# Kernel optimization log

Hardware: AMD Instinct MI355X
Metric: run time of the kernel (lower is better)

The kernel has to match this reference:

```python
import jax, jax.numpy as jnp
import numpy as np

KH, KW = 5, 5
LOWER, UPPER = 0.0, 1.0


def setup_inputs() -> dict:
    key = jax.random.key(0)
    k1, k2, k3, k4, k5, k6, k7 = jax.random.split(key, 7)
    T, Cin, H, W = 15, 64, 256, 256
    Cout, Ho, Wo = 128, 252, 252
    K = 16  # kwta winners
    input_spikes = (jax.random.uniform(k1, (T, Cin, H, W)) < 0.1).astype(jnp.float32)
    output_spikes = (jax.random.uniform(k2, (T, Cout, Ho, Wo)) < 0.05).astype(jnp.float32)
    # winners: distinct feature maps (as produced by k-winners-take-all), valid (r, c)
    f = jax.random.permutation(k3, Cout)[:K]
    r = jax.random.randint(k4, (K,), 0, Ho)
    c = jax.random.randint(k5, (K,), 0, Wo)
    winners = jnp.stack([f, r, c], axis=1).astype(jnp.int64)
    weight = 0.8 + 0.02 * jax.random.normal(k6, (Cout, Cin, KH, KW), dtype=jnp.float32)
    ltp = jnp.full((Cout,), 0.004, dtype=jnp.float32)
    ltd = jnp.full((Cout,), -0.003, dtype=jnp.float32)
    return {"input_spikes": input_spikes, "output_spikes": output_spikes,
            "winners": winners, "weight": weight, "ltp": ltp, "ltd": ltd}


def reference(input_spikes, output_spikes, winners, weight, ltp, ltd):
    # latencies: sum of spikes over time  (Cin,H,W) and (Cout,Ho,Wo)
    in_lat = jnp.sum(input_spikes, axis=0)
    out_lat = jnp.sum(output_spikes, axis=0)
    Cin = in_lat.shape[0]

    def pairing(w):
        f, r, c = w[0], w[1], w[2]
        patch = jax.lax.dynamic_slice(in_lat, (0, r, c), (Cin, KH, KW))  # (Cin,KH,KW)
        return patch >= out_lat[f, r, c]

    pairings = jax.vmap(pairing)(winners)  # (K, Cin, KH, KW) bool
    fs = winners[:, 0]
    lr_rows = jnp.where(pairings,
                        ltp[fs][:, None, None, None],
                        ltd[fs][:, None, None, None])  # (K, Cin, KH, KW)
    lr = jnp.zeros_like(weight).at[fs].set(lr_rows)
    stab = (weight - LOWER) * (UPPER - weight)
    new_weight = weight + lr * stab
    return jnp.clip(new_weight, LOWER, UPPER)
```

## Files before the change

### kernel.cpp

```cpp
#include <hip/hip_runtime.h>

#define T_STEPS 15
#define CIN     64
#define H_IN    256
#define W_IN    256
#define COUT    128
#define HO      252
#define WO      252
#define KWIN    16
#define KH      5
#define KW      5
#define LOWERB  0.0f
#define UPPERB  1.0f

#define W_ELEMS (COUT * CIN * KH * KW)

__global__ __launch_bounds__(256) void stdp_update_kernel(
    const float* __restrict__ in_spikes,
    const float* __restrict__ out_spikes,
    const int*   __restrict__ winners,
    const float* __restrict__ weight,
    const float* __restrict__ ltp,
    const float* __restrict__ ltd,
    float*       __restrict__ out)
{
    __shared__ int   wf[KWIN];
    __shared__ int   wr[KWIN];
    __shared__ int   wc[KWIN];
    __shared__ float wol[KWIN];

    const int tid = threadIdx.x;
    if (tid < KWIN) {
        const int f = winners[3 * tid + 0];
        const int r = winners[3 * tid + 1];
        const int c = winners[3 * tid + 2];
        wf[tid] = f; wr[tid] = r; wc[tid] = c;
        size_t base = (size_t)f * (HO * WO) + (size_t)r * WO + (size_t)c;
        float s = 0.0f;
        #pragma unroll
        for (int t = 0; t < T_STEPS; ++t)
            s += out_spikes[base + (size_t)t * (COUT * HO * WO)];
        wol[tid] = s;
    }
    __syncthreads();

    const int idx = blockIdx.x * blockDim.x + tid;
    if (idx >= W_ELEMS) return;

    const int cout = idx / (CIN * KH * KW);
    const int rem  = idx % (CIN * KH * KW);

    int k = -1;
    #pragma unroll
    for (int i = 0; i < KWIN; ++i)
        if (wf[i] == cout) k = i;

    const float w = weight[idx];
    float nw;
    if (k < 0) {
        nw = w;
    } else {
        const int cin = rem / (KH * KW);
        const int p   = rem % (KH * KW);
        const int kh  = p / KW;
        const int kw  = p % KW;
        const int r   = wr[k] + kh;
        const int c   = wc[k] + kw;
        size_t base = (size_t)cin * (H_IN * W_IN) + (size_t)r * W_IN + (size_t)c;
        float s = 0.0f;
        #pragma unroll
        for (int t = 0; t < T_STEPS; ++t)
            s += in_spikes[base + (size_t)t * (CIN * H_IN * W_IN)];
        const float lr = (s >= wol[k]) ? ltp[cout] : ltd[cout];
        nw = w + lr * ((w - LOWERB) * (UPPERB - w));
    }
    nw = fminf(fmaxf(nw, LOWERB), UPPERB);
    out[idx] = nw;
}

extern "C" void kernel_launch(void* const* d_in, const int* in_sizes, int n_in,
                              void* d_out, int out_size, void* d_ws, size_t ws_size,
                              hipStream_t stream) {
    const float* in_spikes  = (const float*)d_in[0];
    const float* out_spikes = (const float*)d_in[1];
    const int*   winners    = (const int*)d_in[2];
    const float* weight     = (const float*)d_in[3];
    const float* ltp        = (const float*)d_in[4];
    const float* ltd        = (const float*)d_in[5];
    float*       out        = (float*)d_out;

    const int block = 256;
    const int grid  = (W_ELEMS + block - 1) / block;
    stdp_update_kernel<<<grid, block, 0, stream>>>(
        in_spikes, out_spikes, winners, weight, ltp, ltd, out);
}
```

Before: 621.3 us.

## Vectorize weight update to float4 and drop shared-memory winner staging

Each thread now handles four consecutive weights through float4 loads and stores, which cuts the grid by four. The block-wide shared-memory stage that summed winner output latencies is replaced: each thread scans the winners array and, only for winning output channels, computes the output latency itself. This removes a barrier and the 15-step strided out_spikes reads that every block used to do, which dominated the runtime because there are thousands of blocks. The trade-off is that winning threads do redundant out_spikes reads and run four gather loops serially.

```diff
diff --git a/kernel.cpp b/kernel.cpp
--- a/kernel.cpp
+++ b/kernel.cpp
@@ -13,9 +13,11 @@
 #define LOWERB  0.0f
 #define UPPERB  1.0f
 
-#define W_ELEMS (COUT * CIN * KH * KW)
+#define CKK     (CIN * KH * KW)
+#define W_ELEMS (COUT * CKK)
+#define NVEC    (W_ELEMS / 4)
 
-__global__ __launch_bounds__(256) void stdp_update_kernel(
+__global__ __launch_bounds__(256) void stdp_update_v2(
     const float* __restrict__ in_spikes,
     const float* __restrict__ out_spikes,
     const int*   __restrict__ winners,
@@ -24,58 +26,58 @@
     const float* __restrict__ ltd,
     float*       __restrict__ out)
 {
-    __shared__ int   wf[KWIN];
-    __shared__ int   wr[KWIN];
-    __shared__ int   wc[KWIN];
-    __shared__ float wol[KWIN];
+    const int g = blockIdx.x * blockDim.x + threadIdx.x;
+    if (g >= NVEC) return;
+    const int idx  = g * 4;
+    const int cout = idx / CKK;
 
-    const int tid = threadIdx.x;
-    if (tid < KWIN) {
-        const int f = winners[3 * tid + 0];
-        const int r = winners[3 * tid + 1];
-        const int c = winners[3 * tid + 2];
-        wf[tid] = f; wr[tid] = r; wc[tid] = c;
-        size_t base = (size_t)f * (HO * WO) + (size_t)r * WO + (size_t)c;
-        float s = 0.0f;
+    bool win = false;
+    int  wr = 0, wc = 0;
+    #pragma unroll
+    for (int i = 0; i < KWIN; ++i) {
+        const int f = winners[3 * i + 0];
+        const int r = winners[3 * i + 1];
+        const int c = winners[3 * i + 2];
+        if (f == cout) { win = true; wr = r; wc = c; }
+    }
+
+    float4 w = ((const float4*)weight)[g];
+    float* pw = (float*)&w;
+
+    if (win) {
+        float ol = 0.0f;
+        const size_t ob = (size_t)cout * (HO * WO) + (size_t)wr * WO + (size_t)wc;
         #pragma unroll
         for (int t = 0; t < T_STEPS; ++t)
-            s += out_spikes[base + (size_t)t * (COUT * HO * WO)];
-        wol[tid] = s;
+            ol += out_spikes[ob + (size_t)t * (COUT * HO * WO)];
+
+        const float ltpv = ltp[cout];
+        const float ltdv = ltd[cout];
+
+        #pragma unroll
+        for (int j = 0; j < 4; ++j) {
+            const int rem = idx + j - cout * CKK;
+            const int cin = rem / (KH * KW);
+            const int p   = rem % (KH * KW);
+            const int kh  = p / KW;
+            const int kw  = p % KW;
+            const size_t ib = (size_t)cin * (H_IN * W_IN)
+                            + (size_t)(wr + kh) * W_IN + (size_t)(wc + kw);
+            float s = 0.0f;
+            #pragma unroll
+            for (int t = 0; t < T_STEPS; ++t)
+                s += in_spikes[ib + (size_t)t * (CIN * H_IN * W_IN)];
+            const float lr = (s >= ol) ? ltpv : ltdv;
+            const float v  = pw[j];
+            pw[j] = v + lr * ((v - LOWERB) * (UPPERB - v));
+        }
     }
-    __syncthreads();
 
-    const int idx = blockIdx.x * blockDim.x + tid;
-    if (idx >= W_ELEMS) return;
+    #pragma unroll
+    for (int j = 0; j < 4; ++j)
+        pw[j] = fminf(fmaxf(pw[j], LOWERB), UPPERB);
 
-    const int cout = idx / (CIN * KH * KW);
-    const int rem  = idx % (CIN * KH * KW);
-
-    int k = -1;
-    #pragma unroll
-    for (int i = 0; i < KWIN; ++i)
-        if (wf[i] == cout) k = i;
-
-    const float w = weight[idx];
-    float nw;
-    if (k < 0) {
-        nw = w;
-    } else {
-        const int cin = rem / (KH * KW);
-        const int p   = rem % (KH * KW);
-        const int kh  = p / KW;
-        const int kw  = p % KW;
-        const int r   = wr[k] + kh;
-        const int c   = wc[k] + kw;
-        size_t base = (size_t)cin * (H_IN * W_IN) + (size_t)r * W_IN + (size_t)c;
-        float s = 0.0f;
-        #pragma unroll
-        for (int t = 0; t < T_STEPS; ++t)
-            s += in_spikes[base + (size_t)t * (CIN * H_IN * W_IN)];
-        const float lr = (s >= wol[k]) ? ltp[cout] : ltd[cout];
-        nw = w + lr * ((w - LOWERB) * (UPPERB - w));
-    }
-    nw = fminf(fmaxf(nw, LOWERB), UPPERB);
-    out[idx] = nw;
+    ((float4*)out)[g] = w;
 }
 
 extern "C" void kernel_launch(void* const* d_in, const int* in_sizes, int n_in,
@@ -90,7 +92,7 @@
     float*       out        = (float*)d_out;
 
     const int block = 256;
-    const int grid  = (W_ELEMS + block - 1) / block;
-    stdp_update_kernel<<<grid, block, 0, stream>>>(
+    const int grid  = (NVEC + block - 1) / block;
+    stdp_update_v2<<<grid, block, 0, stream>>>(
         in_spikes, out_spikes, winners, weight, ltp, ltd, out);
 }
```

After: 639.6 us. +2.9%, slower.
